# Optimization experiments

Measured on AMD Instinct MI355X. Metric: run time of the kernel, lower is better.

Reference implementation:

```python
import jax, jax.numpy as jnp
import numpy as np

N, K, C = 10000, 64, 128


def setup_inputs() -> dict:
    key = jax.random.key(0)
    ks = jax.random.split(key, 6)
    return {
        "real": jax.random.normal(ks[0], (N, C), dtype=jnp.float32),
        "imag": jax.random.normal(ks[1], (N, C), dtype=jnp.float32),
        "Qreal": jax.random.normal(ks[2], (N, K), dtype=jnp.float32) / np.sqrt(N),
        "Qimag": jax.random.normal(ks[3], (N, K), dtype=jnp.float32) / np.sqrt(N),
        "Ritz": jax.random.uniform(ks[4], (K,), dtype=jnp.float32),
        "weight": jax.random.normal(ks[5], (C, C), dtype=jnp.float32) * np.sqrt(2.0 / (C + C)),  # xavier-ish scale
        "long_diff": 5,
    }


def reference(real, imag, Qreal, Qimag, Ritz, weight, long_diff):
    # TT = Ritz ** long_diff ; spectral filters L = Q diag(TT) Q^H split into real/imag
    TT = jnp.power(Ritz, long_diff)  # [K]
    QrT = Qreal * TT  # [N,K] columns scaled by TT (== Qreal @ diag(TT))
    QiT = Qimag * TT
    L_real = QrT @ Qreal.T + QiT @ Qimag.T  # [N,N]
    L_imag = QiT @ Qreal.T - QrT @ Qimag.T  # [N,N]
    # complex spmm + shared dense weight: (L @ X_complex) @ W
    res_real = (L_real @ real - L_imag @ imag) @ weight  # [N,C]
    res_imag = (L_imag @ real + L_real @ imag) @ weight  # [N,C]
    # complex ReLU: mask by sign of real part
    mask = (res_real >= 0).astype(res_real.dtype)
    return real + mask * res_real, imag + mask * res_imag
```

## Files before the change

### kernel.cpp

```cpp
#include <hip/hip_runtime.h>

#define NN 10000
#define KK 64
#define CC 128
#define OUTOFF (NN * CC)
#define NA 256
#define CHUNKS_A 625

__device__ __forceinline__ float4 f4fma(float s, float4 v, float4 a) {
    a.x = fmaf(s, v.x, a.x); a.y = fmaf(s, v.y, a.y);
    a.z = fmaf(s, v.z, a.z); a.w = fmaf(s, v.w, a.w);
    return a;
}
__device__ __forceinline__ float4 f4add(float4 a, float4 b) {
    a.x += b.x; a.y += b.y; a.z += b.z; a.w += b.w; return a;
}


__global__ __launch_bounds__(512) void kA(const float* __restrict__ re,
                                          const float* __restrict__ im,
                                          const float* __restrict__ Qr,
                                          const float* __restrict__ Qi,
                                          float* __restrict__ part)
{
    __shared__ float4 smem[1536];
    const int t = threadIdx.x;
    const int bid = blockIdx.x;
    const int kt = t & 15;
    const int ctA = t >> 4;
    const int row_q = (t & 255) >> 4, q_q = t & 15;
    const int row_x = t >> 5,          q_x = t & 31;
    const float4* gq  = (const float4*)((t < 256) ? Qr : Qi);
    const float4* gre = (const float4*)re;
    const float4* gim = (const float4*)im;

    float aU[4][4] = {}, aV[4][4] = {};

    int cb = bid;
    float4 r0 = gq [(size_t)(cb * 16 + row_q) * 16 + q_q];
    float4 r1 = gre[(size_t)(cb * 16 + row_x) * 32 + q_x];
    float4 r2 = gim[(size_t)(cb * 16 + row_x) * 32 + q_x];

    while (true) {
        smem[t] = r0; smem[512 + t] = r1; smem[1024 + t] = r2;
        __syncthreads();
        const int nx = cb + NA;
        if (nx < CHUNKS_A) {
            const int m0 = nx * 16;
            r0 = gq [(size_t)(m0 + row_q) * 16 + q_q];
            r1 = gre[(size_t)(m0 + row_x) * 32 + q_x];
            r2 = gim[(size_t)(m0 + row_x) * 32 + q_x];
        }
#pragma unroll 4
        for (int rr = 0; rr < 16; ++rr) {
            float4 q_r = smem[rr * 16 + kt];
            float4 q_i = smem[256 + rr * 16 + kt];
            float4 x_r = smem[512 + rr * 32 + ctA];
            float4 x_i = smem[1024 + rr * 32 + ctA];
            float qr_[4] = {q_r.x, q_r.y, q_r.z, q_r.w};
            float qi_[4] = {q_i.x, q_i.y, q_i.z, q_i.w};
            float xr_[4] = {x_r.x, x_r.y, x_r.z, x_r.w};
            float xi_[4] = {x_i.x, x_i.y, x_i.z, x_i.w};
#pragma unroll
            for (int a = 0; a < 4; ++a)
#pragma unroll
                for (int b = 0; b < 4; ++b) {
                    aU[a][b] = fmaf(qr_[a], xr_[b], aU[a][b]);
                    aU[a][b] = fmaf(qi_[a], xi_[b], aU[a][b]);
                    aV[a][b] = fmaf(qi_[a], xr_[b], aV[a][b]);
                    aV[a][b] = fmaf(-qr_[a], xi_[b], aV[a][b]);
                }
        }
        __syncthreads();
        if (nx >= CHUNKS_A) break;
        cb = nx;
    }
    float* base = part + (size_t)bid * 16384;
    const int k0 = kt * 4, c0 = ctA * 4;
#pragma unroll
    for (int a = 0; a < 4; ++a) {
        *(float4*)(base + (k0 + a) * CC + c0)        = make_float4(aU[a][0], aU[a][1], aU[a][2], aU[a][3]);
        *(float4*)(base + 8192 + (k0 + a) * CC + c0) = make_float4(aV[a][0], aV[a][1], aV[a][2], aV[a][3]);
    }
}

__global__ __launch_bounds__(256) void kRB(const float* __restrict__ part,
                                           const float* __restrict__ Ritz,
                                           const int* __restrict__ ldp,
                                           const float* __restrict__ W,
                                           float* __restrict__ UVW)
{
    __shared__ float4 red4[256];
    __shared__ float rowS[128];
    const int t = threadIdx.x;
    const int m = blockIdx.x >> 6, k = blockIdx.x & 63;
    const int q = t & 31, sl = t >> 5;

    const float4* p = (const float4*)part + (size_t)sl * 4096 + m * 2048 + k * 32 + q;
    float4 z = make_float4(0.f, 0.f, 0.f, 0.f);
    float4 s0 = z, s1 = z, s2 = z, s3 = z;
#pragma unroll 2
    for (int jj = 0; jj < 8; ++jj) {
        s0 = f4add(s0, p[0]);
        s1 = f4add(s1, p[(size_t)8  * 4096]);
        s2 = f4add(s2, p[(size_t)16 * 4096]);
        s3 = f4add(s3, p[(size_t)24 * 4096]);
        p += (size_t)32 * 4096;
    }
    red4[t] = f4add(f4add(s0, s1), f4add(s2, s3));
    __syncthreads();
    if (t < 32) {
        float4 tot = z;
#pragma unroll
        for (int g = 0; g < 8; ++g) tot = f4add(tot, red4[g * 32 + t]);
        ((float4*)rowS)[t] = tot;
    }
    __syncthreads();
    if (t < 128) {
        float acc = 0.f;
#pragma unroll 8
        for (int cp = 0; cp < 128; ++cp)
            acc = fmaf(rowS[cp], W[cp * 128 + t], acc);
        const int ld = *ldp;
        const float rz = Ritz[k];
        float tt = 1.f;
        for (int i = 0; i < ld; ++i) tt *= rz;
        UVW[m * 8192 + k * 128 + t] = tt * acc;
    }
}

__global__ __launch_bounds__(256) void kC(const float* __restrict__ re,
                                          const float* __restrict__ im,
                                          const float* __restrict__ Qr,
                                          const float* __restrict__ Qi,
                                          const float* __restrict__ UVW,
                                          float* __restrict__ out)
{
    __shared__ float4 s[4096];
    const int t = threadIdx.x;
    {
        const float4* g = (const float4*)UVW;
        for (int i = t; i < 4096; i += 256) s[i] = g[i];
    }
    __syncthreads();
    const int ct = t & 31;
    const int r  = t >> 5;
    const int na = blockIdx.x * 16 + r;
    const int nb = na + 8;

    const float4* qra = (const float4*)(Qr + (size_t)na * KK);
    const float4* qia = (const float4*)(Qi + (size_t)na * KK);
    const float4* qrb = (const float4*)(Qr + (size_t)nb * KK);
    const float4* qib = (const float4*)(Qi + (size_t)nb * KK);

    float4 z = make_float4(0.f, 0.f, 0.f, 0.f);
    float4 Ra = z, Ia = z, Rb = z, Ib = z;

#pragma unroll 4
    for (int k4 = 0; k4 < 16; ++k4) {
        float4 QRa = qra[k4], QIa = qia[k4];
        float4 QRb = qrb[k4], QIb = qib[k4];
        float ar[4] = {QRa.x, QRa.y, QRa.z, QRa.w};
        float ai[4] = {QIa.x, QIa.y, QIa.z, QIa.w};
        float br[4] = {QRb.x, QRb.y, QRb.z, QRb.w};
        float bi[4] = {QIb.x, QIb.y, QIb.z, QIb.w};
#pragma unroll
        for (int j = 0; j < 4; ++j) {
            const int k = k4 * 4 + j;
            float4 uw = s[k * 32 + ct];
            float4 vw = s[2048 + k * 32 + ct];
            Ra = f4fma(ar[j], uw, Ra); Ra = f4fma(ai[j], vw, Ra);
            Ia = f4fma(ai[j], uw, Ia); Ia = f4fma(-ar[j], vw, Ia);
            Rb = f4fma(br[j], uw, Rb); Rb = f4fma(bi[j], vw, Rb);
            Ib = f4fma(bi[j], uw, Ib); Ib = f4fma(-br[j], vw, Ib);
        }
    }
    const int cc = ct * 4;
    {
        float4 rin = *(const float4*)(re + (size_t)na * CC + cc);
        float4 iin = *(const float4*)(im + (size_t)na * CC + cc);
        float4 orr, oii;
        orr.x = rin.x + (Ra.x >= 0.f ? Ra.x : 0.f); oii.x = iin.x + (Ra.x >= 0.f ? Ia.x : 0.f);
        orr.y = rin.y + (Ra.y >= 0.f ? Ra.y : 0.f); oii.y = iin.y + (Ra.y >= 0.f ? Ia.y : 0.f);
        orr.z = rin.z + (Ra.z >= 0.f ? Ra.z : 0.f); oii.z = iin.z + (Ra.z >= 0.f ? Ia.z : 0.f);
        orr.w = rin.w + (Ra.w >= 0.f ? Ra.w : 0.f); oii.w = iin.w + (Ra.w >= 0.f ? Ia.w : 0.f);
        *(float4*)(out + (size_t)na * CC + cc)          = orr;
        *(float4*)(out + OUTOFF + (size_t)na * CC + cc) = oii;
    }
    {
        float4 rin = *(const float4*)(re + (size_t)nb * CC + cc);
        float4 iin = *(const float4*)(im + (size_t)nb * CC + cc);
        float4 orr, oii;
        orr.x = rin.x + (Rb.x >= 0.f ? Rb.x : 0.f); oii.x = iin.x + (Rb.x >= 0.f ? Ib.x : 0.f);
        orr.y = rin.y + (Rb.y >= 0.f ? Rb.y : 0.f); oii.y = iin.y + (Rb.y >= 0.f ? Ib.y : 0.f);
        orr.z = rin.z + (Rb.z >= 0.f ? Rb.z : 0.f); oii.z = iin.z + (Rb.z >= 0.f ? Ib.z : 0.f);
        orr.w = rin.w + (Rb.w >= 0.f ? Rb.w : 0.f); oii.w = iin.w + (Rb.w >= 0.f ? Ib.w : 0.f);
        *(float4*)(out + (size_t)nb * CC + cc)          = orr;
        *(float4*)(out + OUTOFF + (size_t)nb * CC + cc) = oii;
    }
}

extern "C" void kernel_launch(void* const* d_in, const int* in_sizes, int n_in,
                              void* d_out, int out_size, void* d_ws, size_t ws_size,
                              hipStream_t stream) {
    const float* re   = (const float*)d_in[0];
    const float* im   = (const float*)d_in[1];
    const float* Qr   = (const float*)d_in[2];
    const float* Qi   = (const float*)d_in[3];
    const float* Ritz = (const float*)d_in[4];
    const float* W    = (const float*)d_in[5];
    const int*   ldp  = (const int*)d_in[6];
    float* out = (float*)d_out;
    float* ws  = (float*)d_ws;

    float* part = ws;
    float* UVW  = ws + (size_t)NA * 16384;

    kA <<<NA,  512, 0, stream>>>(re, im, Qr, Qi, part);
    kRB<<<128, 256, 0, stream>>>(part, Ritz, ldp, W, UVW);
    kC <<<625, 256, 0, stream>>>(re, im, Qr, Qi, UVW, out);
}
```

Before: 113.9 us.

## Fuse three kernels into one persistent kernel with atomic grid barriers

Merges the partial-projection, reduction/weight, and reconstruction kernels into one 256-block persistent kernel. The phases are separated by software grid barriers built on agent-scope atomics, plus a memset to clear the counters each call. The aim is to remove inter-kernel launch gaps and reload the UVW table into shared memory only once per block. In exchange, phase C splits 625 chunks over 512 sub-blocks, so the load is uneven. The barriers also spin-wait and rely on all 256 blocks being co-resident.

```diff
diff --git a/kernel.cpp b/kernel.cpp
--- a/kernel.cpp
+++ b/kernel.cpp
@@ -6,6 +6,7 @@
 #define OUTOFF (NN * CC)
 #define NA 256
 #define CHUNKS_A 625
+#define CHUNKS_C 625
 
 __device__ __forceinline__ float4 f4fma(float s, float4 v, float4 a) {
     a.x = fmaf(s, v.x, a.x); a.y = fmaf(s, v.y, a.y);
@@ -16,187 +17,190 @@
     a.x += b.x; a.y += b.y; a.z += b.z; a.w += b.w; return a;
 }
 
-
-__global__ __launch_bounds__(512) void kA(const float* __restrict__ re,
-                                          const float* __restrict__ im,
-                                          const float* __restrict__ Qr,
-                                          const float* __restrict__ Qi,
-                                          float* __restrict__ part)
+__device__ __forceinline__ void gridbar(unsigned* cnt, unsigned target) {
+    __syncthreads();
+    if (threadIdx.x == 0) {
+        __hip_atomic_fetch_add(cnt, 1u, __ATOMIC_RELEASE, __HIP_MEMORY_SCOPE_AGENT);
+        while (__hip_atomic_load(cnt, __ATOMIC_ACQUIRE, __HIP_MEMORY_SCOPE_AGENT) < target)
+            __builtin_amdgcn_s_sleep(2);
+    }
+    __syncthreads();
+}
+
+
+__global__ __launch_bounds__(512) void fused(
+    const float* __restrict__ re, const float* __restrict__ im,
+    const float* __restrict__ Qr, const float* __restrict__ Qi,
+    const float* __restrict__ Ritz, const int* __restrict__ ldp,
+    const float* __restrict__ W, float* __restrict__ ws,
+    unsigned* __restrict__ cnt, float* __restrict__ out)
 {
-    __shared__ float4 smem[1536];
+    __shared__ float4 smem[4096];
     const int t = threadIdx.x;
     const int bid = blockIdx.x;
-    const int kt = t & 15;
-    const int ctA = t >> 4;
-    const int row_q = (t & 255) >> 4, q_q = t & 15;
-    const int row_x = t >> 5,          q_x = t & 31;
-    const float4* gq  = (const float4*)((t < 256) ? Qr : Qi);
-    const float4* gre = (const float4*)re;
-    const float4* gim = (const float4*)im;
-
-    float aU[4][4] = {}, aV[4][4] = {};
-
-    int cb = bid;
-    float4 r0 = gq [(size_t)(cb * 16 + row_q) * 16 + q_q];
-    float4 r1 = gre[(size_t)(cb * 16 + row_x) * 32 + q_x];
-    float4 r2 = gim[(size_t)(cb * 16 + row_x) * 32 + q_x];
-
-    while (true) {
-        smem[t] = r0; smem[512 + t] = r1; smem[1024 + t] = r2;
-        __syncthreads();
-        const int nx = cb + NA;
-        if (nx < CHUNKS_A) {
-            const int m0 = nx * 16;
-            r0 = gq [(size_t)(m0 + row_q) * 16 + q_q];
-            r1 = gre[(size_t)(m0 + row_x) * 32 + q_x];
-            r2 = gim[(size_t)(m0 + row_x) * 32 + q_x];
-        }
+
+    {
+        const int kt = t & 15;
+        const int ctA = t >> 4;
+        const int row_q = (t & 255) >> 4, q_q = t & 15;
+        const int row_x = t >> 5,          q_x = t & 31;
+        const float4* gq  = (const float4*)((t < 256) ? Qr : Qi);
+        const float4* gre = (const float4*)re;
+        const float4* gim = (const float4*)im;
+
+        float aU[4][4] = {}, aV[4][4] = {};
+
+        int cb = bid;
+        float4 r0 = gq [(size_t)(cb * 16 + row_q) * 16 + q_q];
+        float4 r1 = gre[(size_t)(cb * 16 + row_x) * 32 + q_x];
+        float4 r2 = gim[(size_t)(cb * 16 + row_x) * 32 + q_x];
+
+        while (true) {
+            smem[t] = r0; smem[512 + t] = r1; smem[1024 + t] = r2;
+            __syncthreads();
+            const int nx = cb + NA;
+            if (nx < CHUNKS_A) {
+                const int m0 = nx * 16;
+                r0 = gq [(size_t)(m0 + row_q) * 16 + q_q];
+                r1 = gre[(size_t)(m0 + row_x) * 32 + q_x];
+                r2 = gim[(size_t)(m0 + row_x) * 32 + q_x];
+            }
 #pragma unroll 4
-        for (int rr = 0; rr < 16; ++rr) {
-            float4 q_r = smem[rr * 16 + kt];
-            float4 q_i = smem[256 + rr * 16 + kt];
-            float4 x_r = smem[512 + rr * 32 + ctA];
-            float4 x_i = smem[1024 + rr * 32 + ctA];
-            float qr_[4] = {q_r.x, q_r.y, q_r.z, q_r.w};
-            float qi_[4] = {q_i.x, q_i.y, q_i.z, q_i.w};
-            float xr_[4] = {x_r.x, x_r.y, x_r.z, x_r.w};
-            float xi_[4] = {x_i.x, x_i.y, x_i.z, x_i.w};
-#pragma unroll
-            for (int a = 0; a < 4; ++a)
-#pragma unroll
-                for (int b = 0; b < 4; ++b) {
-                    aU[a][b] = fmaf(qr_[a], xr_[b], aU[a][b]);
-                    aU[a][b] = fmaf(qi_[a], xi_[b], aU[a][b]);
-                    aV[a][b] = fmaf(qi_[a], xr_[b], aV[a][b]);
-                    aV[a][b] = fmaf(-qr_[a], xi_[b], aV[a][b]);
+            for (int rr = 0; rr < 16; ++rr) {
+                float4 q_r = smem[rr * 16 + kt];
+                float4 q_i = smem[256 + rr * 16 + kt];
+                float4 x_r = smem[512 + rr * 32 + ctA];
+                float4 x_i = smem[1024 + rr * 32 + ctA];
+                float qr_[4] = {q_r.x, q_r.y, q_r.z, q_r.w};
+                float qi_[4] = {q_i.x, q_i.y, q_i.z, q_i.w};
+                float xr_[4] = {x_r.x, x_r.y, x_r.z, x_r.w};
+                float xi_[4] = {x_i.x, x_i.y, x_i.z, x_i.w};
+#pragma unroll
+                for (int a = 0; a < 4; ++a)
+#pragma unroll
+                    for (int b = 0; b < 4; ++b) {
+                        aU[a][b] = fmaf(qr_[a], xr_[b], aU[a][b]);
+                        aU[a][b] = fmaf(qi_[a], xi_[b], aU[a][b]);
+                        aV[a][b] = fmaf(qi_[a], xr_[b], aV[a][b]);
+                        aV[a][b] = fmaf(-qr_[a], xi_[b], aV[a][b]);
+                    }
+            }
+            __syncthreads();
+            if (nx >= CHUNKS_A) break;
+            cb = nx;
+        }
+        float* base = ws + (size_t)bid * 16384;
+        const int k0 = kt * 4, c0 = ctA * 4;
+#pragma unroll
+        for (int a = 0; a < 4; ++a) {
+            *(float4*)(base + (k0 + a) * CC + c0)        = make_float4(aU[a][0], aU[a][1], aU[a][2], aU[a][3]);
+            *(float4*)(base + 8192 + (k0 + a) * CC + c0) = make_float4(aV[a][0], aV[a][1], aV[a][2], aV[a][3]);
+        }
+    }
+    gridbar(cnt + 0, NA);
+
+    if (bid < 128) {
+        const int m = bid >> 6, k = bid & 63;
+        const int q = t & 31, sl = t >> 5;
+        const float4* p = (const float4*)ws + (size_t)sl * 4096 + m * 2048 + k * 32 + q;
+        float4 z = make_float4(0.f, 0.f, 0.f, 0.f);
+        float4 s0 = z, s1 = z, s2 = z, s3 = z;
+#pragma unroll
+        for (int jj = 0; jj < 4; ++jj) {
+            s0 = f4add(s0, p[0]);
+            s1 = f4add(s1, p[(size_t)16 * 4096]);
+            s2 = f4add(s2, p[(size_t)32 * 4096]);
+            s3 = f4add(s3, p[(size_t)48 * 4096]);
+            p += (size_t)64 * 4096;
+        }
+        smem[t] = f4add(f4add(s0, s1), f4add(s2, s3));
+        __syncthreads();
+        float* rowS = (float*)(smem + 512);
+        if (t < 32) {
+            float4 tot = make_float4(0.f, 0.f, 0.f, 0.f);
+#pragma unroll
+            for (int g = 0; g < 16; ++g) tot = f4add(tot, smem[g * 32 + t]);
+            ((float4*)rowS)[t] = tot;
+        }
+        __syncthreads();
+        if (t < 128) {
+            float acc = 0.f;
+#pragma unroll 8
+            for (int cp = 0; cp < 128; ++cp)
+                acc = fmaf(rowS[cp], W[cp * 128 + t], acc);
+            const int ld = *ldp;
+            const float rz = Ritz[k];
+            float tt = 1.f;
+            for (int i = 0; i < ld; ++i) tt *= rz;
+            ws[(size_t)NA * 16384 + m * 8192 + k * 128 + t] = tt * acc;
+        }
+        __syncthreads();
+    }
+    gridbar(cnt + 1, NA);
+
+    {
+        const float4* g = (const float4*)(ws + (size_t)NA * 16384);
+        for (int i = t; i < 4096; i += 512) smem[i] = g[i];
+        __syncthreads();
+        const int sub = bid * 2 + (t >> 8);
+        const int tl = t & 255;
+        const int ct = tl & 31;
+        const int r  = tl >> 5;
+
+        for (int cb = sub; cb < CHUNKS_C; cb += 512) {
+            const int na = cb * 16 + r;
+            const int nb = na + 8;
+            const float4* qra = (const float4*)(Qr + (size_t)na * KK);
+            const float4* qia = (const float4*)(Qi + (size_t)na * KK);
+            const float4* qrb = (const float4*)(Qr + (size_t)nb * KK);
+            const float4* qib = (const float4*)(Qi + (size_t)nb * KK);
+
+            float4 z = make_float4(0.f, 0.f, 0.f, 0.f);
+            float4 Ra = z, Ia = z, Rb = z, Ib = z;
+
+#pragma unroll 4
+            for (int k4 = 0; k4 < 16; ++k4) {
+                float4 QRa = qra[k4], QIa = qia[k4];
+                float4 QRb = qrb[k4], QIb = qib[k4];
+                float ar[4] = {QRa.x, QRa.y, QRa.z, QRa.w};
+                float ai[4] = {QIa.x, QIa.y, QIa.z, QIa.w};
+                float br[4] = {QRb.x, QRb.y, QRb.z, QRb.w};
+                float bi[4] = {QIb.x, QIb.y, QIb.z, QIb.w};
+#pragma unroll
+                for (int j = 0; j < 4; ++j) {
+                    const int k = k4 * 4 + j;
+                    float4 uw = smem[k * 32 + ct];
+                    float4 vw = smem[2048 + k * 32 + ct];
+                    Ra = f4fma(ar[j], uw, Ra); Ra = f4fma(ai[j], vw, Ra);
+                    Ia = f4fma(ai[j], uw, Ia); Ia = f4fma(-ar[j], vw, Ia);
+                    Rb = f4fma(br[j], uw, Rb); Rb = f4fma(bi[j], vw, Rb);
+                    Ib = f4fma(bi[j], uw, Ib); Ib = f4fma(-br[j], vw, Ib);
                 }
-        }
-        __syncthreads();
-        if (nx >= CHUNKS_A) break;
-        cb = nx;
-    }
-    float* base = part + (size_t)bid * 16384;
-    const int k0 = kt * 4, c0 = ctA * 4;
-#pragma unroll
-    for (int a = 0; a < 4; ++a) {
-        *(float4*)(base + (k0 + a) * CC + c0)        = make_float4(aU[a][0], aU[a][1], aU[a][2], aU[a][3]);
-        *(float4*)(base + 8192 + (k0 + a) * CC + c0) = make_float4(aV[a][0], aV[a][1], aV[a][2], aV[a][3]);
-    }
-}
-
-__global__ __launch_bounds__(256) void kRB(const float* __restrict__ part,
-                                           const float* __restrict__ Ritz,
-                                           const int* __restrict__ ldp,
-                                           const float* __restrict__ W,
-                                           float* __restrict__ UVW)
-{
-    __shared__ float4 red4[256];
-    __shared__ float rowS[128];
-    const int t = threadIdx.x;
-    const int m = blockIdx.x >> 6, k = blockIdx.x & 63;
-    const int q = t & 31, sl = t >> 5;
-
-    const float4* p = (const float4*)part + (size_t)sl * 4096 + m * 2048 + k * 32 + q;
-    float4 z = make_float4(0.f, 0.f, 0.f, 0.f);
-    float4 s0 = z, s1 = z, s2 = z, s3 = z;
-#pragma unroll 2
-    for (int jj = 0; jj < 8; ++jj) {
-        s0 = f4add(s0, p[0]);
-        s1 = f4add(s1, p[(size_t)8  * 4096]);
-        s2 = f4add(s2, p[(size_t)16 * 4096]);
-        s3 = f4add(s3, p[(size_t)24 * 4096]);
-        p += (size_t)32 * 4096;
-    }
-    red4[t] = f4add(f4add(s0, s1), f4add(s2, s3));
-    __syncthreads();
-    if (t < 32) {
-        float4 tot = z;
-#pragma unroll
-        for (int g = 0; g < 8; ++g) tot = f4add(tot, red4[g * 32 + t]);
-        ((float4*)rowS)[t] = tot;
-    }
-    __syncthreads();
-    if (t < 128) {
-        float acc = 0.f;
-#pragma unroll 8
-        for (int cp = 0; cp < 128; ++cp)
-            acc = fmaf(rowS[cp], W[cp * 128 + t], acc);
-        const int ld = *ldp;
-        const float rz = Ritz[k];
-        float tt = 1.f;
-        for (int i = 0; i < ld; ++i) tt *= rz;
-        UVW[m * 8192 + k * 128 + t] = tt * acc;
-    }
-}
-
-__global__ __launch_bounds__(256) void kC(const float* __restrict__ re,
-                                          const float* __restrict__ im,
-                                          const float* __restrict__ Qr,
-                                          const float* __restrict__ Qi,
-                                          const float* __restrict__ UVW,
-                                          float* __restrict__ out)
-{
-    __shared__ float4 s[4096];
-    const int t = threadIdx.x;
-    {
-        const float4* g = (const float4*)UVW;
-        for (int i = t; i < 4096; i += 256) s[i] = g[i];
-    }
-    __syncthreads();
-    const int ct = t & 31;
-    const int r  = t >> 5;
-    const int na = blockIdx.x * 16 + r;
-    const int nb = na + 8;
-
-    const float4* qra = (const float4*)(Qr + (size_t)na * KK);
-    const float4* qia = (const float4*)(Qi + (size_t)na * KK);
-    const float4* qrb = (const float4*)(Qr + (size_t)nb * KK);
-    const float4* qib = (const float4*)(Qi + (size_t)nb * KK);
-
-    float4 z = make_float4(0.f, 0.f, 0.f, 0.f);
-    float4 Ra = z, Ia = z, Rb = z, Ib = z;
-
-#pragma unroll 4
-    for (int k4 = 0; k4 < 16; ++k4) {
-        float4 QRa = qra[k4], QIa = qia[k4];
-        float4 QRb = qrb[k4], QIb = qib[k4];
-        float ar[4] = {QRa.x, QRa.y, QRa.z, QRa.w};
-        float ai[4] = {QIa.x, QIa.y, QIa.z, QIa.w};
-        float br[4] = {QRb.x, QRb.y, QRb.z, QRb.w};
-        float bi[4] = {QIb.x, QIb.y, QIb.z, QIb.w};
-#pragma unroll
-        for (int j = 0; j < 4; ++j) {
-            const int k = k4 * 4 + j;
-            float4 uw = s[k * 32 + ct];
-            float4 vw = s[2048 + k * 32 + ct];
-            Ra = f4fma(ar[j], uw, Ra); Ra = f4fma(ai[j], vw, Ra);
-            Ia = f4fma(ai[j], uw, Ia); Ia = f4fma(-ar[j], vw, Ia);
-            Rb = f4fma(br[j], uw, Rb); Rb = f4fma(bi[j], vw, Rb);
-            Ib = f4fma(bi[j], uw, Ib); Ib = f4fma(-br[j], vw, Ib);
-        }
-    }
-    const int cc = ct * 4;
-    {
-        float4 rin = *(const float4*)(re + (size_t)na * CC + cc);
-        float4 iin = *(const float4*)(im + (size_t)na * CC + cc);
-        float4 orr, oii;
-        orr.x = rin.x + (Ra.x >= 0.f ? Ra.x : 0.f); oii.x = iin.x + (Ra.x >= 0.f ? Ia.x : 0.f);
-        orr.y = rin.y + (Ra.y >= 0.f ? Ra.y : 0.f); oii.y = iin.y + (Ra.y >= 0.f ? Ia.y : 0.f);
-        orr.z = rin.z + (Ra.z >= 0.f ? Ra.z : 0.f); oii.z = iin.z + (Ra.z >= 0.f ? Ia.z : 0.f);
-        orr.w = rin.w + (Ra.w >= 0.f ? Ra.w : 0.f); oii.w = iin.w + (Ra.w >= 0.f ? Ia.w : 0.f);
-        *(float4*)(out + (size_t)na * CC + cc)          = orr;
-        *(float4*)(out + OUTOFF + (size_t)na * CC + cc) = oii;
-    }
-    {
-        float4 rin = *(const float4*)(re + (size_t)nb * CC + cc);
-        float4 iin = *(const float4*)(im + (size_t)nb * CC + cc);
-        float4 orr, oii;
-        orr.x = rin.x + (Rb.x >= 0.f ? Rb.x : 0.f); oii.x = iin.x + (Rb.x >= 0.f ? Ib.x : 0.f);
-        orr.y = rin.y + (Rb.y >= 0.f ? Rb.y : 0.f); oii.y = iin.y + (Rb.y >= 0.f ? Ib.y : 0.f);
-        orr.z = rin.z + (Rb.z >= 0.f ? Rb.z : 0.f); oii.z = iin.z + (Rb.z >= 0.f ? Ib.z : 0.f);
-        orr.w = rin.w + (Rb.w >= 0.f ? Rb.w : 0.f); oii.w = iin.w + (Rb.w >= 0.f ? Ib.w : 0.f);
-        *(float4*)(out + (size_t)nb * CC + cc)          = orr;
-        *(float4*)(out + OUTOFF + (size_t)nb * CC + cc) = oii;
+            }
+            const int cc = ct * 4;
+            {
+                float4 rin = *(const float4*)(re + (size_t)na * CC + cc);
+                float4 iin = *(const float4*)(im + (size_t)na * CC + cc);
+                float4 orr, oii;
+                orr.x = rin.x + (Ra.x >= 0.f ? Ra.x : 0.f); oii.x = iin.x + (Ra.x >= 0.f ? Ia.x : 0.f);
+                orr.y = rin.y + (Ra.y >= 0.f ? Ra.y : 0.f); oii.y = iin.y + (Ra.y >= 0.f ? Ia.y : 0.f);
+                orr.z = rin.z + (Ra.z >= 0.f ? Ra.z : 0.f); oii.z = iin.z + (Ra.z >= 0.f ? Ia.z : 0.f);
+                orr.w = rin.w + (Ra.w >= 0.f ? Ra.w : 0.f); oii.w = iin.w + (Ra.w >= 0.f ? Ia.w : 0.f);
+                *(float4*)(out + (size_t)na * CC + cc)          = orr;
+                *(float4*)(out + OUTOFF + (size_t)na * CC + cc) = oii;
+            }
+            {
+                float4 rin = *(const float4*)(re + (size_t)nb * CC + cc);
+                float4 iin = *(const float4*)(im + (size_t)nb * CC + cc);
+                float4 orr, oii;
+                orr.x = rin.x + (Rb.x >= 0.f ? Rb.x : 0.f); oii.x = iin.x + (Rb.x >= 0.f ? Ib.x : 0.f);
+                orr.y = rin.y + (Rb.y >= 0.f ? Rb.y : 0.f); oii.y = iin.y + (Rb.y >= 0.f ? Ib.y : 0.f);
+                orr.z = rin.z + (Rb.z >= 0.f ? Rb.z : 0.f); oii.z = iin.z + (Rb.z >= 0.f ? Ib.z : 0.f);
+                orr.w = rin.w + (Rb.w >= 0.f ? Rb.w : 0.f); oii.w = iin.w + (Rb.w >= 0.f ? Ib.w : 0.f);
+                *(float4*)(out + (size_t)nb * CC + cc)          = orr;
+                *(float4*)(out + OUTOFF + (size_t)nb * CC + cc) = oii;
+            }
+        }
     }
 }
 
@@ -213,10 +217,13 @@
     float* out = (float*)d_out;
     float* ws  = (float*)d_ws;
 
-    float* part = ws;
-    float* UVW  = ws + (size_t)NA * 16384;
-
-    kA <<<NA,  512, 0, stream>>>(re, im, Qr, Qi, part);
-    kRB<<<128, 256, 0, stream>>>(part, Ritz, ldp, W, UVW);
-    kC <<<625, 256, 0, stream>>>(re, im, Qr, Qi, UVW, out);
-}
+    unsigned* cnt = (unsigned*)(ws + (size_t)NA * 16384 + 16384);
+    hipMemsetAsync((void*)cnt, 0, 16, stream);
+
+    void* kargs[] = { (void*)&re, (void*)&im, (void*)&Qr, (void*)&Qi,
+                      (void*)&Ritz, (void*)&ldp, (void*)&W, (void*)&ws,
+                      (void*)&cnt, (void*)&out };
+    hipLaunchKernelGGL(fused, dim3(NA), dim3(512), 0, stream,
+                       re, im, Qr, Qi, Ritz, ldp, W, ws, cnt, out);
+    (void)kargs;
+}
```

Measured after the change: 162.5 us. 1.43x slower.

## Rebalance kA chunking to 20-row chunks and widen kRB reduction to 512 threads

Applied to the files above, without the earlier changes.

Changes the first-stage reduction kernel from 625 chunks of 16 rows to 500 chunks of 20 rows. The 256 blocks then process at most two chunks each instead of three, which shortens the critical path. Shared-memory staging is generalized with per-thread source tables so four load slots cover the larger tile. The partial-sum reduction kernel doubles its thread count to read more partial slices in parallel. This adds some index setup and a predicated fourth load.

```diff
diff --git a/kernel.cpp b/kernel.cpp
--- a/kernel.cpp
+++ b/kernel.cpp
@@ -5,7 +5,8 @@
 #define CC 128
 #define OUTOFF (NN * CC)
 #define NA 256
-#define CHUNKS_A 625
+#define ROWS_A 20
+#define CHUNKS_A 500
 
 __device__ __forceinline__ float4 f4fma(float s, float4 v, float4 a) {
     a.x = fmaf(s, v.x, a.x); a.y = fmaf(s, v.y, a.y);
@@ -23,40 +24,54 @@
                                           const float* __restrict__ Qi,
                                           float* __restrict__ part)
 {
-    __shared__ float4 smem[1536];
+    __shared__ float4 smem[1920];
     const int t = threadIdx.x;
     const int bid = blockIdx.x;
     const int kt = t & 15;
-    const int ctA = t >> 4;
-    const int row_q = (t & 255) >> 4, q_q = t & 15;
-    const int row_x = t >> 5,          q_x = t & 31;
-    const float4* gq  = (const float4*)((t < 256) ? Qr : Qi);
-    const float4* gre = (const float4*)re;
-    const float4* gim = (const float4*)im;
+    const int ct = t >> 4;
+
+    const float4* gp[4];
+    int str[4], rc[4];
+#pragma unroll
+    for (int s = 0; s < 4; ++s) {
+        const int f = t + 512 * s;
+        if (f < 320)       { gp[s] = (const float4*)Qr; str[s] = 16; rc[s] = f; }
+        else if (f < 640)  { gp[s] = (const float4*)Qi; str[s] = 16; rc[s] = f - 320; }
+        else if (f < 1280) { gp[s] = (const float4*)re; str[s] = 32; rc[s] = f - 640; }
+        else               { gp[s] = (const float4*)im; str[s] = 32; rc[s] = f - 1280; }
+    }
+    const bool has3 = (t < 1920 - 1536);
 
     float aU[4][4] = {}, aV[4][4] = {};
 
     int cb = bid;
-    float4 r0 = gq [(size_t)(cb * 16 + row_q) * 16 + q_q];
-    float4 r1 = gre[(size_t)(cb * 16 + row_x) * 32 + q_x];
-    float4 r2 = gim[(size_t)(cb * 16 + row_x) * 32 + q_x];
+    float4 r0, r1, r2, r3;
+    {
+        const int n0 = cb * ROWS_A;
+        r0 = gp[0][(size_t)n0 * str[0] + rc[0]];
+        r1 = gp[1][(size_t)n0 * str[1] + rc[1]];
+        r2 = gp[2][(size_t)n0 * str[2] + rc[2]];
+        if (has3) r3 = gp[3][(size_t)n0 * str[3] + rc[3]];
+    }
 
     while (true) {
         smem[t] = r0; smem[512 + t] = r1; smem[1024 + t] = r2;
+        if (has3) smem[1536 + t] = r3;
         __syncthreads();
         const int nx = cb + NA;
         if (nx < CHUNKS_A) {
-            const int m0 = nx * 16;
-            r0 = gq [(size_t)(m0 + row_q) * 16 + q_q];
-            r1 = gre[(size_t)(m0 + row_x) * 32 + q_x];
-            r2 = gim[(size_t)(m0 + row_x) * 32 + q_x];
+            const int n0 = nx * ROWS_A;
+            r0 = gp[0][(size_t)n0 * str[0] + rc[0]];
+            r1 = gp[1][(size_t)n0 * str[1] + rc[1]];
+            r2 = gp[2][(size_t)n0 * str[2] + rc[2]];
+            if (has3) r3 = gp[3][(size_t)n0 * str[3] + rc[3]];
         }
 #pragma unroll 4
-        for (int rr = 0; rr < 16; ++rr) {
+        for (int rr = 0; rr < ROWS_A; ++rr) {
             float4 q_r = smem[rr * 16 + kt];
-            float4 q_i = smem[256 + rr * 16 + kt];
-            float4 x_r = smem[512 + rr * 32 + ctA];
-            float4 x_i = smem[1024 + rr * 32 + ctA];
+            float4 q_i = smem[320 + rr * 16 + kt];
+            float4 x_r = smem[640 + rr * 32 + ct];
+            float4 x_i = smem[1280 + rr * 32 + ct];
             float qr_[4] = {q_r.x, q_r.y, q_r.z, q_r.w};
             float qi_[4] = {q_i.x, q_i.y, q_i.z, q_i.w};
             float xr_[4] = {x_r.x, x_r.y, x_r.z, x_r.w};
@@ -76,7 +91,7 @@
         cb = nx;
     }
     float* base = part + (size_t)bid * 16384;
-    const int k0 = kt * 4, c0 = ctA * 4;
+    const int k0 = kt * 4, c0 = ct * 4;
 #pragma unroll
     for (int a = 0; a < 4; ++a) {
         *(float4*)(base + (k0 + a) * CC + c0)        = make_float4(aU[a][0], aU[a][1], aU[a][2], aU[a][3]);
@@ -84,13 +99,13 @@
     }
 }
 
-__global__ __launch_bounds__(256) void kRB(const float* __restrict__ part,
+__global__ __launch_bounds__(512) void kRB(const float* __restrict__ part,
                                            const float* __restrict__ Ritz,
                                            const int* __restrict__ ldp,
                                            const float* __restrict__ W,
                                            float* __restrict__ UVW)
 {
-    __shared__ float4 red4[256];
+    __shared__ float4 red4[512];
     __shared__ float rowS[128];
     const int t = threadIdx.x;
     const int m = blockIdx.x >> 6, k = blockIdx.x & 63;
@@ -99,20 +114,20 @@
     const float4* p = (const float4*)part + (size_t)sl * 4096 + m * 2048 + k * 32 + q;
     float4 z = make_float4(0.f, 0.f, 0.f, 0.f);
     float4 s0 = z, s1 = z, s2 = z, s3 = z;
-#pragma unroll 2
-    for (int jj = 0; jj < 8; ++jj) {
+#pragma unroll
+    for (int jj = 0; jj < 4; ++jj) {
         s0 = f4add(s0, p[0]);
-        s1 = f4add(s1, p[(size_t)8  * 4096]);
-        s2 = f4add(s2, p[(size_t)16 * 4096]);
-        s3 = f4add(s3, p[(size_t)24 * 4096]);
-        p += (size_t)32 * 4096;
+        s1 = f4add(s1, p[(size_t)16 * 4096]);
+        s2 = f4add(s2, p[(size_t)32 * 4096]);
+        s3 = f4add(s3, p[(size_t)48 * 4096]);
+        p += (size_t)64 * 4096;
     }
     red4[t] = f4add(f4add(s0, s1), f4add(s2, s3));
     __syncthreads();
     if (t < 32) {
         float4 tot = z;
 #pragma unroll
-        for (int g = 0; g < 8; ++g) tot = f4add(tot, red4[g * 32 + t]);
+        for (int g = 0; g < 16; ++g) tot = f4add(tot, red4[g * 32 + t]);
         ((float4*)rowS)[t] = tot;
     }
     __syncthreads();
@@ -217,6 +232,6 @@
     float* UVW  = ws + (size_t)NA * 16384;
 
     kA <<<NA,  512, 0, stream>>>(re, im, Qr, Qi, part);
-    kRB<<<128, 256, 0, stream>>>(part, Ritz, ldp, W, UVW);
+    kRB<<<128, 512, 0, stream>>>(part, Ritz, ldp, W, UVW);
     kC <<<625, 256, 0, stream>>>(re, im, Qr, Qi, UVW, out);
 }
```

New measurement: 116.0 us. About the same (+1.8%).
